# Kernel tuning notes

Hardware: AMD Instinct MI355X
Metric: run time of the kernel (lower is better)

The kernel has to match this reference:

```python
import jax, jax.numpy as jnp
import numpy as np

IOU_LOW = 0.5   # <= low  -> background (-1)
IOU_HIGH = 0.6  # (low, high) -> neutral (-1e8)
NEUTRAL = -1e8


def setup_inputs() -> dict:
    key = jax.random.key(0)
    k1, k2, k3, k4, k5 = jax.random.split(key, 5)
    B, N, M = 16, 32768, 64
    # Proposals: XYXY boxes inside an ~800x800 image (built from rand fills).
    p_xy1 = jax.random.uniform(k1, (B, N, 2), dtype=jnp.float32) * 600.0
    p_wh = jax.random.uniform(k2, (B, N, 2), dtype=jnp.float32) * 200.0 + 1.0
    proposals = jnp.concatenate([p_xy1, p_xy1 + p_wh], axis=-1)  # (B, N, 4)
    # GT boxes: XYXY + float class id in last column (all valid here; the
    # reference still implements the class==-1 padding mask like the torch code).
    g_xy1 = jax.random.uniform(k3, (B, M, 2), dtype=jnp.float32) * 600.0
    g_wh = jax.random.uniform(k4, (B, M, 2), dtype=jnp.float32) * 200.0 + 1.0
    g_cls = jax.random.randint(k5, (B, M, 1), 0, 20).astype(jnp.float32)
    gt_boxes = jnp.concatenate([g_xy1, g_xy1 + g_wh, g_cls], axis=-1)  # (B, M, 5)
    return {"proposals": proposals, "gt_boxes": gt_boxes}


def _pairwise_iou(b1, b2):
    # b1: (N, 4), b2: (M, 4), XYXY -> (N, M)
    area1 = (b1[:, 2] - b1[:, 0]) * (b1[:, 3] - b1[:, 1])  # (N,)
    area2 = (b2[:, 2] - b2[:, 0]) * (b2[:, 3] - b2[:, 1])  # (M,)
    x1 = jnp.maximum(b1[:, None, 0], b2[None, :, 0])
    y1 = jnp.maximum(b1[:, None, 1], b2[None, :, 1])
    x2 = jnp.minimum(b1[:, None, 2], b2[None, :, 2])
    y2 = jnp.minimum(b1[:, None, 3], b2[None, :, 3])
    inter = jnp.maximum(x2 - x1, 0.0) * jnp.maximum(y2 - y1, 0.0)
    return inter / (area1[:, None] + area2[None, :] - inter)


def _match_one(props, gtb):
    # props: (N, 4), gtb: (M, 5) with class==-1 marking padded GT boxes.
    valid = gtb[:, 4] != -1.0  # (M,)
    iou = _pairwise_iou(props, gtb[:, :4])  # (N, M)
    iou = jnp.where(valid[None, :], iou, -1.0)
    match_quality = jnp.max(iou, axis=1)  # (N,)
    matched_idxs = jnp.argmax(iou, axis=1)  # (N,)
    matched = gtb[matched_idxs]  # (N, 5) gather of boxes+class
    matched = jnp.where((match_quality <= IOU_LOW)[:, None], -1.0, matched)
    neutral = (match_quality > IOU_LOW) & (match_quality < IOU_HIGH)
    matched = jnp.where(neutral[:, None], NEUTRAL, matched)
    # No valid GT at all -> all background (fake boxes/class = -1).
    matched = jnp.where(jnp.any(valid), matched, -1.0)
    return matched


def reference(proposals, gt_boxes):
    # proposals: (B, N, 4), gt_boxes: (B, M, 5) -> matched GT (B, N, 5)
    return jax.vmap(_match_one)(proposals, gt_boxes)
```

## Files before the change

kernel.cpp:

```cpp
#include <hip/hip_runtime.h>

#define BATCH 16
#define NPROP 32768
#define NGT   64
#define BLOCK 256

__global__ __launch_bounds__(BLOCK) void rcnn_match_kernel(
    const float* __restrict__ props,
    const float* __restrict__ gt,
    float* __restrict__ out)
{
    __shared__ float sgt[NGT][8];

    const int blocksPerBatch = NPROP / BLOCK;
    const int b = blockIdx.x / blocksPerBatch;
    const int n = (blockIdx.x % blocksPerBatch) * BLOCK + threadIdx.x;

    if (threadIdx.x < NGT) {
        const float* g = gt + ((size_t)b * NGT + threadIdx.x) * 5;
        float x1 = g[0], y1 = g[1], x2 = g[2], y2 = g[3], c = g[4];
        float a2 = (x2 - x1) * (y2 - y1);
        if (c == -1.0f) { x1 = y1 = x2 = y2 = -1.0e4f; a2 = 1.0f; }
        sgt[threadIdx.x][0] = x1;
        sgt[threadIdx.x][1] = y1;
        sgt[threadIdx.x][2] = x2;
        sgt[threadIdx.x][3] = y2;
        sgt[threadIdx.x][4] = c;
        sgt[threadIdx.x][5] = a2;
    }
    __syncthreads();

    const float4 p = reinterpret_cast<const float4*>(props)[(size_t)b * NPROP + n];
    const float area1 = (p.z - p.x) * (p.w - p.y);

    float bestNum = -1.0f;
    float bestDen = 1.0f;
    int   besti   = 0;

    #pragma unroll 8
    for (int m = 0; m < NGT; ++m) {
        const float gx1 = sgt[m][0];
        const float gy1 = sgt[m][1];
        const float gx2 = sgt[m][2];
        const float gy2 = sgt[m][3];
        const float a2  = sgt[m][5];

        const float ix1 = fmaxf(p.x, gx1);
        const float iy1 = fmaxf(p.y, gy1);
        const float ix2 = fminf(p.z, gx2);
        const float iy2 = fminf(p.w, gy2);
        const float inter = fmaxf(ix2 - ix1, 0.0f) * fmaxf(iy2 - iy1, 0.0f);
        const float den   = (area1 + a2) - inter;

        const bool better = inter * bestDen > bestNum * den;
        bestNum = better ? inter : bestNum;
        bestDen = better ? den   : bestDen;
        besti   = better ? m     : besti;
    }

    const float q = bestNum / bestDen;

    float o0, o1, o2, o3, o4;
    if (q <= 0.5f) {
        o0 = o1 = o2 = o3 = o4 = -1.0f;
    } else if (q < 0.6f) {
        o0 = o1 = o2 = o3 = o4 = -1.0e8f;
    } else {
        o0 = sgt[besti][0];
        o1 = sgt[besti][1];
        o2 = sgt[besti][2];
        o3 = sgt[besti][3];
        o4 = sgt[besti][4];
    }

    float* op = out + ((size_t)b * NPROP + n) * 5;
    op[0] = o0; op[1] = o1; op[2] = o2; op[3] = o3; op[4] = o4;
}

extern "C" void kernel_launch(void* const* d_in, const int* in_sizes, int n_in,
                              void* d_out, int out_size, void* d_ws, size_t ws_size,
                              hipStream_t stream) {
    const float* props = (const float*)d_in[0];
    const float* gt    = (const float*)d_in[1];
    float* out = (float*)d_out;

    const int grid = BATCH * (NPROP / BLOCK);
    rcnn_match_kernel<<<grid, BLOCK, 0, stream>>>(props, gt, out);
}
```

Baseline: 24.07 us.

## Precompute cleaned GT boxes in a prep kernel and read them via scalar loads

Adds a small prep kernel that writes sanitized GT boxes and their areas into workspace. The match kernel then reads them straight from global memory with uniform indices, which should compile to scalar loads, instead of staging them through LDS behind a block barrier. The final gather reads the original GT. This removes the per-block LDS fill and __syncthreads, and the unroll factor goes from 8 to 16. In exchange it adds a second kernel launch and depends on the scalar cache holding the GT data.

```diff
diff --git a/kernel.cpp b/kernel.cpp
--- a/kernel.cpp
+++ b/kernel.cpp
@@ -5,45 +5,44 @@
 #define NGT   64
 #define BLOCK 256
 
-__global__ __launch_bounds__(BLOCK) void rcnn_match_kernel(
+__global__ void prep_kernel(const float* __restrict__ gt, float* __restrict__ ws) {
+    const int t = blockIdx.x * blockDim.x + threadIdx.x;
+    if (t >= BATCH * NGT) return;
+    const float* g = gt + (size_t)t * 5;
+    float x1 = g[0], y1 = g[1], x2 = g[2], y2 = g[3], c = g[4];
+    float a2 = (x2 - x1) * (y2 - y1);
+    if (c == -1.0f) { x1 = y1 = x2 = y2 = -1.0e4f; a2 = 1.0f; }
+    float* w = ws + (size_t)t * 8;
+    w[0] = x1; w[1] = y1; w[2] = x2; w[3] = y2;
+    w[4] = a2; w[5] = c;  w[6] = 0.f; w[7] = 0.f;
+}
+
+__global__ __launch_bounds__(BLOCK) void match_kernel(
     const float* __restrict__ props,
     const float* __restrict__ gt,
+    const float* __restrict__ cln,
     float* __restrict__ out)
 {
-    __shared__ float sgt[NGT][8];
-
     const int blocksPerBatch = NPROP / BLOCK;
     const int b = blockIdx.x / blocksPerBatch;
     const int n = (blockIdx.x % blocksPerBatch) * BLOCK + threadIdx.x;
 
-    if (threadIdx.x < NGT) {
-        const float* g = gt + ((size_t)b * NGT + threadIdx.x) * 5;
-        float x1 = g[0], y1 = g[1], x2 = g[2], y2 = g[3], c = g[4];
-        float a2 = (x2 - x1) * (y2 - y1);
-        if (c == -1.0f) { x1 = y1 = x2 = y2 = -1.0e4f; a2 = 1.0f; }
-        sgt[threadIdx.x][0] = x1;
-        sgt[threadIdx.x][1] = y1;
-        sgt[threadIdx.x][2] = x2;
-        sgt[threadIdx.x][3] = y2;
-        sgt[threadIdx.x][4] = c;
-        sgt[threadIdx.x][5] = a2;
-    }
-    __syncthreads();
-
     const float4 p = reinterpret_cast<const float4*>(props)[(size_t)b * NPROP + n];
     const float area1 = (p.z - p.x) * (p.w - p.y);
+
+    const float* cb = cln + (size_t)b * NGT * 8;
 
     float bestNum = -1.0f;
     float bestDen = 1.0f;
     int   besti   = 0;
 
-    #pragma unroll 8
+    #pragma unroll 16
     for (int m = 0; m < NGT; ++m) {
-        const float gx1 = sgt[m][0];
-        const float gy1 = sgt[m][1];
-        const float gx2 = sgt[m][2];
-        const float gy2 = sgt[m][3];
-        const float a2  = sgt[m][5];
+        const float gx1 = cb[m * 8 + 0];
+        const float gy1 = cb[m * 8 + 1];
+        const float gx2 = cb[m * 8 + 2];
+        const float gy2 = cb[m * 8 + 3];
+        const float a2  = cb[m * 8 + 4];
 
         const float ix1 = fmaxf(p.x, gx1);
         const float iy1 = fmaxf(p.y, gy1);
@@ -66,11 +65,8 @@
     } else if (q < 0.6f) {
         o0 = o1 = o2 = o3 = o4 = -1.0e8f;
     } else {
-        o0 = sgt[besti][0];
-        o1 = sgt[besti][1];
-        o2 = sgt[besti][2];
-        o3 = sgt[besti][3];
-        o4 = sgt[besti][4];
+        const float* g0 = gt + ((size_t)b * NGT + besti) * 5;
+        o0 = g0[0]; o1 = g0[1]; o2 = g0[2]; o3 = g0[3]; o4 = g0[4];
     }
 
     float* op = out + ((size_t)b * NPROP + n) * 5;
@@ -83,7 +79,10 @@
     const float* props = (const float*)d_in[0];
     const float* gt    = (const float*)d_in[1];
     float* out = (float*)d_out;
+    float* cln = (float*)d_ws;
+
+    prep_kernel<<<(BATCH * NGT + BLOCK - 1) / BLOCK, BLOCK, 0, stream>>>(gt, cln);
 
     const int grid = BATCH * (NPROP / BLOCK);
-    rcnn_match_kernel<<<grid, BLOCK, 0, stream>>>(props, gt, out);
+    match_kernel<<<grid, BLOCK, 0, stream>>>(props, gt, cln, out);
 }
```

After: 32.21 us. 1.34x slower.

## Process four proposals per thread to reuse GT shared-memory loads

Applied to the files above, without the earlier changes.

Each thread now handles four proposals strided by the block size, so every GT box read from LDS is reused across four IoU computations. The GT row is read as one float4 vector load, with area and class swapped into slots 4 and 5 to make this possible. The output selection becomes branchless. The grid shrinks by four, which on this problem size leaves 512 blocks and may reduce latency hiding and occupancy.

```diff
diff --git a/kernel.cpp b/kernel.cpp
--- a/kernel.cpp
+++ b/kernel.cpp
@@ -4,17 +4,18 @@
 #define NPROP 32768
 #define NGT   64
 #define BLOCK 256
+#define P     4
 
-__global__ __launch_bounds__(BLOCK) void rcnn_match_kernel(
+__global__ __launch_bounds__(BLOCK) void match_kernel(
     const float* __restrict__ props,
     const float* __restrict__ gt,
     float* __restrict__ out)
 {
     __shared__ float sgt[NGT][8];
 
-    const int blocksPerBatch = NPROP / BLOCK;
-    const int b = blockIdx.x / blocksPerBatch;
-    const int n = (blockIdx.x % blocksPerBatch) * BLOCK + threadIdx.x;
+    const int blocksPerBatch = NPROP / (BLOCK * P);
+    const int b    = blockIdx.x / blocksPerBatch;
+    const int base = (blockIdx.x % blocksPerBatch) * (BLOCK * P);
 
     if (threadIdx.x < NGT) {
         const float* g = gt + ((size_t)b * NGT + threadIdx.x) * 5;
@@ -25,56 +26,64 @@
         sgt[threadIdx.x][1] = y1;
         sgt[threadIdx.x][2] = x2;
         sgt[threadIdx.x][3] = y2;
-        sgt[threadIdx.x][4] = c;
-        sgt[threadIdx.x][5] = a2;
+        sgt[threadIdx.x][4] = a2;
+        sgt[threadIdx.x][5] = c;
     }
     __syncthreads();
 
-    const float4 p = reinterpret_cast<const float4*>(props)[(size_t)b * NPROP + n];
-    const float area1 = (p.z - p.x) * (p.w - p.y);
+    const float4* pv = reinterpret_cast<const float4*>(props)
+                     + (size_t)b * NPROP + base + threadIdx.x;
+    float4 p[P];
+    float  a1[P];
+    #pragma unroll
+    for (int k = 0; k < P; ++k) {
+        p[k]  = pv[k * BLOCK];
+        a1[k] = (p[k].z - p[k].x) * (p[k].w - p[k].y);
+    }
 
-    float bestNum = -1.0f;
-    float bestDen = 1.0f;
-    int   besti   = 0;
+    float bn[P], bd[P];
+    int   bi[P];
+    #pragma unroll
+    for (int k = 0; k < P; ++k) { bn[k] = -1.0f; bd[k] = 1.0f; bi[k] = 0; }
 
     #pragma unroll 8
     for (int m = 0; m < NGT; ++m) {
-        const float gx1 = sgt[m][0];
-        const float gy1 = sgt[m][1];
-        const float gx2 = sgt[m][2];
-        const float gy2 = sgt[m][3];
-        const float a2  = sgt[m][5];
+        const float4 g  = *reinterpret_cast<const float4*>(&sgt[m][0]);
+        const float  a2 = sgt[m][4];
+        #pragma unroll
+        for (int k = 0; k < P; ++k) {
+            const float ix1 = fmaxf(p[k].x, g.x);
+            const float iy1 = fmaxf(p[k].y, g.y);
+            const float ix2 = fminf(p[k].z, g.z);
+            const float iy2 = fminf(p[k].w, g.w);
+            const float inter = fmaxf(ix2 - ix1, 0.0f) * fmaxf(iy2 - iy1, 0.0f);
+            const float den   = (a1[k] + a2) - inter;
 
-        const float ix1 = fmaxf(p.x, gx1);
-        const float iy1 = fmaxf(p.y, gy1);
-        const float ix2 = fminf(p.z, gx2);
-        const float iy2 = fminf(p.w, gy2);
-        const float inter = fmaxf(ix2 - ix1, 0.0f) * fmaxf(iy2 - iy1, 0.0f);
-        const float den   = (area1 + a2) - inter;
-
-        const bool better = inter * bestDen > bestNum * den;
-        bestNum = better ? inter : bestNum;
-        bestDen = better ? den   : bestDen;
-        besti   = better ? m     : besti;
+            const bool better = inter * bd[k] > bn[k] * den;
+            bn[k] = better ? inter : bn[k];
+            bd[k] = better ? den   : bd[k];
+            bi[k] = better ? m     : bi[k];
+        }
     }
 
-    const float q = bestNum / bestDen;
+    #pragma unroll
+    for (int k = 0; k < P; ++k) {
+        const float q = bn[k] / bd[k];
+        const float4 g  = *reinterpret_cast<const float4*>(&sgt[bi[k]][0]);
+        const float  gc = sgt[bi[k]][5];
 
-    float o0, o1, o2, o3, o4;
-    if (q <= 0.5f) {
-        o0 = o1 = o2 = o3 = o4 = -1.0f;
-    } else if (q < 0.6f) {
-        o0 = o1 = o2 = o3 = o4 = -1.0e8f;
-    } else {
-        o0 = sgt[besti][0];
-        o1 = sgt[besti][1];
-        o2 = sgt[besti][2];
-        o3 = sgt[besti][3];
-        o4 = sgt[besti][4];
+        const bool bg      = (q <= 0.5f);
+        const bool neutral = (q > 0.5f) & (q < 0.6f);
+        const float fill   = neutral ? -1.0e8f : -1.0f;
+        const bool keep    = !(bg | neutral);
+
+        float* op = out + ((size_t)b * NPROP + base + threadIdx.x + k * BLOCK) * 5;
+        op[0] = keep ? g.x : fill;
+        op[1] = keep ? g.y : fill;
+        op[2] = keep ? g.z : fill;
+        op[3] = keep ? g.w : fill;
+        op[4] = keep ? gc  : fill;
     }
-
-    float* op = out + ((size_t)b * NPROP + n) * 5;
-    op[0] = o0; op[1] = o1; op[2] = o2; op[3] = o3; op[4] = o4;
 }
 
 extern "C" void kernel_launch(void* const* d_in, const int* in_sizes, int n_in,
@@ -84,6 +93,6 @@
     const float* gt    = (const float*)d_in[1];
     float* out = (float*)d_out;
 
-    const int grid = BATCH * (NPROP / BLOCK);
-    rcnn_match_kernel<<<grid, BLOCK, 0, stream>>>(props, gt, out);
+    const int grid = BATCH * (NPROP / (BLOCK * P));
+    match_kernel<<<grid, BLOCK, 0, stream>>>(props, gt, out);
 }
```

New measurement: 23.45 us. -2.6%, faster.
